# Optimization experiments

Hardware: AMD Instinct MI355X
Metric: run time of the kernel (lower is better)

The kernel has to match this reference:

```python
import jax, jax.numpy as jnp
import numpy as np

N_R, N_U, N_P = 40000, 30000, 30000
N = N_R + N_U + N_P
E = 1600000
NFEAT, NHID, NCLASS = 128, 128, 40


def setup_inputs() -> dict:
    key = jax.random.key(0)
    ks = jax.random.split(key, 12)
    s = 0.05
    return {
        "inputx_r": jax.random.normal(ks[0], (N_R, 5), jnp.float32),
        "inputx_u": jax.random.normal(ks[1], (N_U, 7), jnp.float32),
        "inputx_p": jax.random.normal(ks[2], (N_P, 6), jnp.float32),
        "edge_index": jax.random.randint(ks[3], (2, E), 0, N, jnp.int64)
            if jax.config.jax_enable_x64 else jax.random.randint(ks[3], (2, E), 0, N, jnp.int32),
        "W_r": jax.random.normal(ks[4], (5, NFEAT), jnp.float32) * s,
        "b_r": jax.random.normal(ks[5], (NFEAT,), jnp.float32) * s,
        "W_u": jax.random.normal(ks[6], (7, NFEAT), jnp.float32) * s,
        "b_u": jax.random.normal(ks[7], (NFEAT,), jnp.float32) * s,
        "W_p": jax.random.normal(ks[8], (6, NFEAT), jnp.float32) * s,
        "b_p": jax.random.normal(ks[9], (NFEAT,), jnp.float32) * s,
        "W1": jax.random.normal(ks[10], (NFEAT, NHID), jnp.float32) * s,
        "W2": jax.random.normal(ks[11], (NHID, NCLASS), jnp.float32) * s,
    }


def _gcn_conv(x, W, src, dst, num_nodes):
    # GCNConv(add_self_loops=False, normalize=False, bias=False):
    # out = A @ (x @ W), unit edge weights, aggregation at dst of source messages.
    h = x @ W                                      # [N, d_out]
    return jax.ops.segment_sum(h[src], dst, num_segments=num_nodes)


def reference(inputx_r, inputx_u, inputx_p, edge_index,
              W_r, b_r, W_u, b_u, W_p, b_p, W1, W2):
    # Segment-wise input projections (nums = [[N_R, N_R+N_U], [.,.], [.,.]]
    # with empty 2nd/3rd blocks; tail is the p-segment), then two GCN layers.
    x = jnp.concatenate([
        inputx_r @ W_r + b_r,   # nodes [0 : N_R]
        inputx_u @ W_u + b_u,   # nodes [N_R : N_R+N_U]
        inputx_p @ W_p + b_p,   # nodes [N_R+N_U : N]
    ], axis=0)                  # [N, NFEAT]
    src, dst = edge_index[0], edge_index[1]
    h = jax.nn.relu(_gcn_conv(x, W1, src, dst, N))   # gc1 + relu
    # dropout: inference (training=False) -> identity
    out = _gcn_conv(h, W2, src, dst, N)              # gc2
    return out
```

## Files before the change

### kernel.cpp

```cpp
#include <hip/hip_runtime.h>

constexpr int kNR = 40000;
constexpr int kNU = 30000;
constexpr int kNP = 30000;
constexpr int kN  = 100000;
constexpr int kE  = 1600000;
constexpr int kF  = 128;
constexpr int kC  = 40;
constexpr int kBN = 64;
constexpr int kNB = (kN + kBN - 1) / kBN;
constexpr int kNBp = 1600;
constexpr int kCH = 256;
constexpr int kCE = kE / kCH;
constexpr int kSlot = 2048;
constexpr int kPackB = 196;
constexpr int kSetupB = kPackB + 2;

typedef __attribute__((ext_vector_type(8))) short bf16x8;
typedef __attribute__((ext_vector_type(4))) float f32x4;

__device__ __forceinline__ float bf_to_f(unsigned short h) {
    union { unsigned int i; float f; } u; u.i = ((unsigned int)h) << 16; return u.f;
}
__device__ __forceinline__ unsigned short f_to_bf(float f) {
    union { unsigned int i; float f; } u; u.f = f;
    unsigned int r = u.i + 0x7FFFu + ((u.i >> 16) & 1u);
    return (unsigned short)(r >> 16);
}
__device__ __forceinline__ float2 bf2_to_f2(unsigned int p) {
    union { unsigned int i; float f; } lo, hi;
    lo.i = (p & 0xFFFFu) << 16;
    hi.i = p & 0xFFFF0000u;
    return make_float2(lo.f, hi.f);
}
__device__ __forceinline__ unsigned int pack_bf2(float a, float b) {
    return (unsigned int)f_to_bf(a) | ((unsigned int)f_to_bf(b) << 16);
}
__device__ __forceinline__ float ldf(const void* p, int i, int isbf) {
    return isbf ? bf_to_f(((const unsigned short*)p)[i]) : ((const float*)p)[i];
}
__device__ __forceinline__ int lde(const int* p, int i, int is64) {
    return is64 ? p[2 * i] : p[i];
}

__device__ __forceinline__ int sniff_isbf(const void* W1, int t, int* sh) {
    if (t < 64) {
        unsigned int wv = ((const unsigned int*)W1)[t];
        unsigned int ax = wv & 0x7FFFu;
        int pl = (ax == 0u) || (ax > 0x2000u && ax < 0x4000u);
        unsigned long long mk = __ballot(pl);
        if (t == 0) *sh = (__popcll(mk) >= 48) ? 1 : 0;
    }
    __syncthreads();
    return *sh;
}

__global__ void __launch_bounds__(512) gcn_setup(
        const void* __restrict__ xr, const void* __restrict__ xu, const void* __restrict__ xp,
        const void* __restrict__ Wr, const void* __restrict__ br,
        const void* __restrict__ Wu, const void* __restrict__ bu,
        const void* __restrict__ Wp, const void* __restrict__ bp,
        const void* __restrict__ W1, const void* __restrict__ W2,
        unsigned short* __restrict__ fwfrag, unsigned short* __restrict__ w2frag,
        uint4* __restrict__ xpack, int* __restrict__ gcnt) {
    __shared__ __align__(16) char smem[29696];
    __shared__ int sisbf;
    int t = threadIdx.x;
    int bx = blockIdx.x;
    int isbf = sniff_isbf(W1, t, &sisbf);
    if (bx < kPackB) {
        int n = bx * 512 + t;
        if (n >= kN) return;
        const void* base; int roff, d;
        if (n < kNR)            { base = xr; roff = n * 5;               d = 5; }
        else if (n < kNR + kNU) { base = xu; roff = (n - kNR) * 7;       d = 7; }
        else                    { base = xp; roff = (n - kNR - kNU) * 6; d = 6; }
        float f[8];
        #pragma unroll
        for (int i = 0; i < 8; i++) f[i] = (i < d) ? ldf(base, roff + i, isbf) : 0.f;
        uint4 u;
        u.x = pack_bf2(f[0], f[1]);  u.y = pack_bf2(f[2], f[3]);
        u.z = pack_bf2(f[4], f[5]);  u.w = pack_bf2(f[6], f[7]);
        xpack[n] = u;
    } else if (bx == kPackB) {
        float* sw   = (float*)smem;
        float* pacc = (float*)(smem + 10752);
        unsigned short* flds = (unsigned short*)(smem + 21504);
        for (int i = t; i < 21 * kF; i += 512) {
            int r = i >> 7, c = i & 127;
            float v;
            if (r < 5)        v = ldf(Wr, r * kF + c, isbf);
            else if (r < 12)  v = ldf(Wu, (r - 5) * kF + c, isbf);
            else if (r < 18)  v = ldf(Wp, (r - 12) * kF + c, isbf);
            else if (r == 18) v = ldf(br, c, isbf);
            else if (r == 19) v = ldf(bu, c, isbf);
            else              v = ldf(bp, c, isbf);
            sw[i] = v;
        }
        __syncthreads();
        {
            bool active = (t < 256);
            int j = t & 127, half = (t >> 7) & 1;
            float acc[21];
            #pragma unroll
            for (int r = 0; r < 21; r++) acc[r] = 0.f;
            if (active) {
                int k0 = half * 64, k1 = k0 + 64;
                for (int k = k0; k < k1; k++) {
                    float w1 = ldf(W1, k * kF + j, isbf);
                    #pragma unroll
                    for (int r = 0; r < 21; r++) acc[r] += sw[r * kF + k] * w1;
                }
            }
            if (active && half == 1) {
                #pragma unroll
                for (int r = 0; r < 21; r++) pacc[r * kF + j] = acc[r];
            }
            __syncthreads();
            if (active && half == 0) {
                #pragma unroll
                for (int r = 0; r < 21; r++) acc[r] += pacc[r * kF + j];
                unsigned short row[32];
                #pragma unroll
                for (int s = 0; s < 32; s++) row[s] = 0;
                #pragma unroll
                for (int i = 0; i < 5; i++) row[0  + i] = f_to_bf(acc[i]);
                #pragma unroll
                for (int i = 0; i < 7; i++) row[8  + i] = f_to_bf(acc[5 + i]);
                #pragma unroll
                for (int i = 0; i < 6; i++) row[16 + i] = f_to_bf(acc[12 + i]);
                row[24] = f_to_bf(acc[18]);  row[25] = f_to_bf(acc[19]);  row[26] = f_to_bf(acc[20]);
                #pragma unroll
                for (int s = 0; s < 32; s++) flds[j * 32 + s] = row[s];
            }
        }
        __syncthreads();
        for (int idx = t; idx < 8 * 64; idx += 512) {
            int t8 = idx >> 6, lane = idx & 63;
            int mm = lane & 15, q = lane >> 4;
            #pragma unroll
            for (int j = 0; j < 8; j++)
                fwfrag[idx * 8 + j] = flds[(16 * t8 + mm) * 32 + q * 8 + j];
        }
    } else {
        for (int i = t; i < kNBp; i += 512) gcnt[i] = 0;
        for (int idx = t; idx < 12 * 64; idx += 512) {
            int st = idx >> 6, lane = idx & 63;
            int s = st / 3, tt = st % 3;
            int mm = lane & 15, q = lane >> 4;
            int cls = 16 * tt + mm;
            #pragma unroll
            for (int j = 0; j < 8; j++) {
                int k = s * 32 + q * 8 + j;
                w2frag[idx * 8 + j] = (cls < kC) ? f_to_bf(ldf(W2, k * kC + cls, isbf))
                                                 : (unsigned short)0;
            }
        }
    }
}

__global__ void __launch_bounds__(1024) gcn_scatter(const int* __restrict__ ei,
                                                    int* __restrict__ gcnt,
                                                    unsigned int* __restrict__ slots) {
    __shared__ int hist[kNBp];
    __shared__ int cur[kNBp];
    __shared__ int sis64;
    int t = threadIdx.x;
    int blk = blockIdx.x;
    if (t < 64) {
        int v = ((const int*)ei)[2 * t + 1];
        unsigned long long mk = __ballot(v != 0);
        if (t == 0) sis64 = (mk == 0ull) ? 1 : 0;
    }
    for (int i = t; i < kNBp; i += 1024) hist[i] = 0;
    __syncthreads();
    int is64 = sis64;
    int e0 = blk * kCE, e1 = e0 + kCE;
    for (int eb = e0 + t; eb < e1; eb += 4096) {
        unsigned int d[4]; int ok[4];
        #pragma unroll
        for (int j = 0; j < 4; j++) {
            int e = eb + j * 1024;
            ok[j] = (e < e1);
            d[j] = ok[j] ? (unsigned int)lde(ei, kE + e, is64) : 0xFFFFFFFFu;
        }
        #pragma unroll
        for (int j = 0; j < 4; j++)
            if (d[j] < (unsigned int)kN) atomicAdd(&hist[d[j] >> 6], 1);
    }
    __syncthreads();
    int off = (blk * 401) % kNBp;
    for (int j = t; j < kNBp; j += 1024) {
        int i = j + off;
        if (i >= kNBp) i -= kNBp;
        int h = hist[i];
        cur[i] = (h > 0) ? atomicAdd(&gcnt[i], h) : 0;
    }
    __syncthreads();
    for (int eb = e0 + t; eb < e1; eb += 4096) {
        unsigned int d[4], s[4]; int ok[4];
        #pragma unroll
        for (int j = 0; j < 4; j++) {
            int e = eb + j * 1024;
            ok[j] = (e < e1);
            d[j] = ok[j] ? (unsigned int)lde(ei, kE + e, is64) : 0xFFFFFFFFu;
        }
        #pragma unroll
        for (int j = 0; j < 4; j++) {
            int e = eb + j * 1024;
            s[j] = ok[j] ? (unsigned int)lde(ei, e, is64) : 0u;
        }
        #pragma unroll
        for (int j = 0; j < 4; j++) {
            if (d[j] < (unsigned int)kN) {
                unsigned int sv = (s[j] < (unsigned int)kN) ? s[j] : 0u;
                int b = (int)(d[j] >> 6);
                int pos = atomicAdd(&cur[b], 1);
                if (pos < kSlot) slots[(size_t)b * kSlot + pos] = (sv << 6) | (d[j] & 63u);
            }
        }
    }
}

__global__ void __launch_bounds__(256) GCN_2190433321521_kernel(
        const unsigned int* __restrict__ slots,
        const int* __restrict__ gcnt,
        const uint4* __restrict__ xpack,
        const unsigned short* __restrict__ fwfrag,
        const unsigned short* __restrict__ w2frag,
        int* __restrict__ rpb,
        int* __restrict__ rpe,
        int* __restrict__ col,
        unsigned short* __restrict__ hw) {
    __shared__ __align__(16) char smem[25600];
    float*          agg_l  = (float*)smem;
    int*            cnt_l  = (int*)(smem + 7424);
    int*            strt_l = (int*)(smem + 7680);
    int*            cntv_l = (int*)(smem + 7936);
    unsigned int*   wst    = (unsigned int*)(smem + 8192);
    int*            col_l  = (int*)(smem + 16384);
    unsigned short* hbuf   = (unsigned short*)(smem + 8192);

    int b = blockIdx.x;
    int base = b * kBN;
    int nn = min(kBN, kN - base);
    int tid = threadIdx.x;

    if (tid < kBN) cnt_l[tid] = 0;
    __syncthreads();
    int p0 = b * kSlot;
    int m = min(gcnt[b], kSlot);
    int p1 = p0 + m;

    for (int ib = p0 + tid; ib < p1; ib += 1024) {
        unsigned int w[4]; int ok[4];
        #pragma unroll
        for (int j = 0; j < 4; j++) {
            int i = ib + j * 256;
            ok[j] = (i < p1);
            w[j] = ok[j] ? slots[i] : 0u;
        }
        #pragma unroll
        for (int j = 0; j < 4; j++) {
            int i = ib + j * 256;
            if (ok[j]) {
                wst[i - p0] = w[j];
                atomicAdd(&cnt_l[w[j] & 63u], 1);
            }
        }
    }
    __syncthreads();
    if (tid < 64) {
        int v = cnt_l[tid];
        int incl = v;
        #pragma unroll
        for (int o = 1; o < 64; o <<= 1) {
            int y = __shfl_up(incl, o, 64);
            if (tid >= o) incl += y;
        }
        int cursor = p0 + incl - v;
        cnt_l[tid]  = cursor;
        strt_l[tid] = cursor;
        cntv_l[tid] = v;
        if (tid < nn) { rpb[base + tid] = cursor; rpe[base + tid] = cursor + v; }
    }
    __syncthreads();

    for (int i = p0 + tid; i < p1; i += 256) {
        unsigned int w = wst[i - p0];
        unsigned int s = w >> 6;
        int dloc = (int)(w & 63u);
        int pos = atomicAdd(&cnt_l[dloc], 1);
        col_l[pos - p0] = (int)s;
    }
    __syncthreads();
    for (int i = tid; i < m; i += 256) col[p0 + i] = col_l[i];

    {
        int node = tid >> 2, j = tid & 3;
        float aR[8], aU[8], aP[8];
        #pragma unroll
        for (int i = 0; i < 8; i++) { aR[i] = 0.f; aU[i] = 0.f; aP[i] = 0.f; }
        float cR = 0.f, cU = 0.f, cP = 0.f;
        int start = strt_l[node] - p0;
        int c = cntv_l[node];
        for (int i = start + j; i < start + c; i += 4) {
            int s = col_l[i];
            uint4 u = xpack[s];
            float2 q0 = bf2_to_f2(u.x), q1 = bf2_to_f2(u.y);
            float2 q2 = bf2_to_f2(u.z), q3 = bf2_to_f2(u.w);
            if (s < kNR) {
                aR[0]+=q0.x; aR[1]+=q0.y; aR[2]+=q1.x; aR[3]+=q1.y;
                aR[4]+=q2.x; aR[5]+=q2.y; aR[6]+=q3.x; aR[7]+=q3.y; cR += 1.f;
            } else if (s < kNR + kNU) {
                aU[0]+=q0.x; aU[1]+=q0.y; aU[2]+=q1.x; aU[3]+=q1.y;
                aU[4]+=q2.x; aU[5]+=q2.y; aU[6]+=q3.x; aU[7]+=q3.y; cU += 1.f;
            } else {
                aP[0]+=q0.x; aP[1]+=q0.y; aP[2]+=q1.x; aP[3]+=q1.y;
                aP[4]+=q2.x; aP[5]+=q2.y; aP[6]+=q3.x; aP[7]+=q3.y; cP += 1.f;
            }
        }
        #pragma unroll
        for (int i = 0; i < 8; i++) {
            float v = aR[i];
            v += __shfl_xor(v, 1, 64);  v += __shfl_xor(v, 2, 64);
            if (j == 0) agg_l[node * 29 + i] = v;
        }
        #pragma unroll
        for (int i = 0; i < 8; i++) {
            float v = aU[i];
            v += __shfl_xor(v, 1, 64);  v += __shfl_xor(v, 2, 64);
            if (j == 0) agg_l[node * 29 + 8 + i] = v;
        }
        #pragma unroll
        for (int i = 0; i < 8; i++) {
            float v = aP[i];
            v += __shfl_xor(v, 1, 64);  v += __shfl_xor(v, 2, 64);
            if (j == 0) agg_l[node * 29 + 16 + i] = v;
        }
        float v = cR;
        v += __shfl_xor(v, 1, 64);  v += __shfl_xor(v, 2, 64);
        if (j == 0) agg_l[node * 29 + 24] = v;
        v = cU;
        v += __shfl_xor(v, 1, 64);  v += __shfl_xor(v, 2, 64);
        if (j == 0) agg_l[node * 29 + 25] = v;
        v = cP;
        v += __shfl_xor(v, 1, 64);  v += __shfl_xor(v, 2, 64);
        if (j == 0) agg_l[node * 29 + 26] = v;
    }
    __syncthreads();

    int wid = tid >> 6, lane = tid & 63;
    int mm = lane & 15, q = lane >> 4;
    int node = wid * 16 + mm;
    bf16x8 a1;
    #pragma unroll
    for (int j = 0; j < 8; j++) {
        int sl = q * 8 + j;
        a1[j] = (sl < 27) ? (short)f_to_bf(agg_l[node * 29 + sl]) : (short)0;
    }
    const bf16x8* fwf = (const bf16x8*)fwfrag;
    f32x4 c1[8];
    #pragma unroll
    for (int t = 0; t < 8; t++) {
        f32x4 z = {0.f, 0.f, 0.f, 0.f};
        c1[t] = __builtin_amdgcn_mfma_f32_16x16x32_bf16(a1, fwf[t * 64 + lane], z, 0, 0, 0);
    }
    unsigned short* hb = hbuf + wid * 16 * 136;
    #pragma unroll
    for (int t = 0; t < 8; t++) {
        #pragma unroll
        for (int r = 0; r < 4; r++)
            hb[(q * 4 + r) * 136 + 16 * t + mm] = f_to_bf(fmaxf(c1[t][r], 0.f));
    }
    const bf16x8* w2f = (const bf16x8*)w2frag;
    f32x4 c2[3];
    #pragma unroll
    for (int t = 0; t < 3; t++) { c2[t].x = 0.f; c2[t].y = 0.f; c2[t].z = 0.f; c2[t].w = 0.f; }
    #pragma unroll
    for (int s = 0; s < 4; s++) {
        bf16x8 a2 = *(const bf16x8*)&hb[mm * 136 + s * 32 + q * 8];
        #pragma unroll
        for (int t = 0; t < 3; t++)
            c2[t] = __builtin_amdgcn_mfma_f32_16x16x32_bf16(a2, w2f[(s * 3 + t) * 64 + lane],
                                                            c2[t], 0, 0, 0);
    }
    #pragma unroll
    for (int t = 0; t < 3; t++) {
        int cls = 16 * t + mm;
        if (cls < kC) {
            #pragma unroll
            for (int r = 0; r < 4; r++) {
                int n = base + wid * 16 + q * 4 + r;
                if (n < kN) hw[(size_t)n * kC + cls] = f_to_bf(c2[t][r]);
            }
        }
    }
}

__global__ void __launch_bounds__(256) gcn_gather2(const unsigned int* __restrict__ hw32,
                                                   const int* __restrict__ rpb,
                                                   const int* __restrict__ rpe,
                                                   const int* __restrict__ col,
                                                   unsigned int* __restrict__ out,
                                                   const void* __restrict__ W1) {
    __shared__ int sisbf;
    int t = threadIdx.x;
    int isbf = sniff_isbf(W1, t, &sisbf);
    int w = (blockIdx.x * 256 + t) >> 6;
    if (w >= kN) return;
    int lane = t & 63;
    int grp = lane / 10;
    int c2  = lane % 10;
    int beg = rpb[w], end = rpe[w];
    float f0 = 0.f, f1 = 0.f, f2 = 0.f, f3 = 0.f;
    if (grp < 6) {
        const uint2* hp = (const uint2*)hw32;
        int e = beg + grp;
        for (; e + 6 < end; e += 12) {
            int s0 = col[e], s1 = col[e + 6];
            uint2 v0 = hp[s0 * 10 + c2];
            uint2 v1 = hp[s1 * 10 + c2];
            float2 a0 = bf2_to_f2(v0.x), b0 = bf2_to_f2(v0.y);
            float2 a1 = bf2_to_f2(v1.x), b1 = bf2_to_f2(v1.y);
            f0 += a0.x + a1.x;  f1 += a0.y + a1.y;
            f2 += b0.x + b1.x;  f3 += b0.y + b1.y;
        }
        if (e < end) {
            uint2 v = hp[col[e] * 10 + c2];
            float2 a = bf2_to_f2(v.x), bb = bf2_to_f2(v.y);
            f0 += a.x; f1 += a.y; f2 += bb.x; f3 += bb.y;
        }
    }
    f0 += __shfl(f0, lane + 30, 64);
    f1 += __shfl(f1, lane + 30, 64);
    f2 += __shfl(f2, lane + 30, 64);
    f3 += __shfl(f3, lane + 30, 64);
    f0 += __shfl(f0, lane + 10, 64) + __shfl(f0, lane + 20, 64);
    f1 += __shfl(f1, lane + 10, 64) + __shfl(f1, lane + 20, 64);
    f2 += __shfl(f2, lane + 10, 64) + __shfl(f2, lane + 20, 64);
    f3 += __shfl(f3, lane + 10, 64) + __shfl(f3, lane + 20, 64);
    if (lane < 10) {
        if (isbf) {
            out[w * 20 + 2 * lane]     = pack_bf2(f0, f1);
            out[w * 20 + 2 * lane + 1] = pack_bf2(f2, f3);
        } else {
            float* of = (float*)out;
            of[w * 40 + 4 * lane]     = f0;
            of[w * 40 + 4 * lane + 1] = f1;
            of[w * 40 + 4 * lane + 2] = f2;
            of[w * 40 + 4 * lane + 3] = f3;
        }
    }
}

extern "C" void kernel_launch(void* const* d_in, const int* in_sizes, int n_in,
                              void* d_out, int out_size, void* d_ws, size_t ws_size,
                              hipStream_t stream) {
    const void* xr = d_in[0];
    const void* xu = d_in[1];
    const void* xp = d_in[2];
    const int*  ei = (const int*)d_in[3];
    const void* Wr = d_in[4];
    const void* br = d_in[5];
    const void* Wu = d_in[6];
    const void* bu = d_in[7];
    const void* Wp = d_in[8];
    const void* bp = d_in[9];
    const void* W1 = d_in[10];
    const void* W2 = d_in[11];
    (void)in_sizes; (void)n_in; (void)out_size; (void)ws_size;

    char* ws = (char*)d_ws;
    size_t off = 0;
    auto alloc = [&](size_t bytes) -> void* {
        void* p = (void*)(ws + off);
        off = (off + bytes + 255) & ~(size_t)255;
        return p;
    };
    int*            gcnt   = (int*)           alloc((size_t)kNBp * 4);
    unsigned short* fwfrag = (unsigned short*)alloc(8 * 64 * 8 * 2);
    unsigned short* w2frag = (unsigned short*)alloc(12 * 64 * 8 * 2);
    uint4*          xpack  = (uint4*)         alloc((size_t)kN * 16);
    unsigned int*   slots  = (unsigned int*)  alloc((size_t)kNB * kSlot * 4);
    int*            col    = (int*)           alloc((size_t)kNB * kSlot * 4);
    int*            rpb    = (int*)           alloc((size_t)kN * 4);
    int*            rpe    = (int*)           alloc((size_t)kN * 4);
    unsigned short* hwb    = (unsigned short*)alloc((size_t)kN * kC * 2);

    gcn_setup<<<kSetupB, 512, 0, stream>>>(xr, xu, xp, Wr, br, Wu, bu, Wp, bp, W1, W2,
                                           fwfrag, w2frag, xpack, gcnt);
    gcn_scatter<<<kCH, 1024, 0, stream>>>(ei, gcnt, slots);
    GCN_2190433321521_kernel<<<kNB, 256, 0, stream>>>(slots, gcnt, xpack, fwfrag, w2frag,
                                                      rpb, rpe, col, hwb);
    gcn_gather2<<<(kN * 64 + 255) / 256, 256, 0, stream>>>((const unsigned int*)hwb, rpb, rpe,
                                                           col, (unsigned int*)d_out, W1);
}
```

Measured before the change: 190.7 us.

## Merge setup and scatter kernels, stage layer-2 outputs in LDS, prefetch gather indices

Folds the setup kernel and the edge-scatter kernel into one launch with 1024-thread blocks, and moves the counter zeroing to a memset. This removes a kernel boundary and lets the scatter run alongside the packing work. The main kernel now writes its layer-2 bf16 outputs to shared memory first, then stores them to global memory as contiguous 32-bit words. The second gather preloads four column indices up front to expose more memory-level parallelism. The cost is an extra memset launch, extra block syncs, and halving the scatter block count, which may reduce parallelism in the edge pass.

```diff
diff --git a/kernel.cpp b/kernel.cpp
--- a/kernel.cpp
+++ b/kernel.cpp
@@ -10,11 +10,14 @@
 constexpr int kBN = 64;
 constexpr int kNB = (kN + kBN - 1) / kBN;
 constexpr int kNBp = 1600;
-constexpr int kCH = 256;
-constexpr int kCE = kE / kCH;
 constexpr int kSlot = 2048;
-constexpr int kPackB = 196;
-constexpr int kSetupB = kPackB + 2;
+constexpr int kPackB = 98;
+constexpr int kFuseB = kPackB;
+constexpr int kW2B   = kPackB + 1;
+constexpr int kScat0 = kPackB + 2;
+constexpr int kScatB = 128;
+constexpr int kCE    = kE / kScatB;
+constexpr int kPrepB = kScat0 + kScatB;
 
 typedef __attribute__((ext_vector_type(8))) short bf16x8;
 typedef __attribute__((ext_vector_type(4))) float f32x4;
@@ -55,21 +58,23 @@
     return *sh;
 }
 
-__global__ void __launch_bounds__(512) gcn_setup(
+__global__ void __launch_bounds__(1024) gcn_prep(
         const void* __restrict__ xr, const void* __restrict__ xu, const void* __restrict__ xp,
         const void* __restrict__ Wr, const void* __restrict__ br,
         const void* __restrict__ Wu, const void* __restrict__ bu,
         const void* __restrict__ Wp, const void* __restrict__ bp,
         const void* __restrict__ W1, const void* __restrict__ W2,
+        const int* __restrict__ ei,
         unsigned short* __restrict__ fwfrag, unsigned short* __restrict__ w2frag,
-        uint4* __restrict__ xpack, int* __restrict__ gcnt) {
+        uint4* __restrict__ xpack, int* __restrict__ gcnt,
+        unsigned int* __restrict__ slots) {
     __shared__ __align__(16) char smem[29696];
-    __shared__ int sisbf;
+    __shared__ int sflag;
     int t = threadIdx.x;
     int bx = blockIdx.x;
-    int isbf = sniff_isbf(W1, t, &sisbf);
     if (bx < kPackB) {
-        int n = bx * 512 + t;
+        int isbf = sniff_isbf(W1, t, &sflag);
+        int n = bx * 1024 + t;
         if (n >= kN) return;
         const void* base; int roff, d;
         if (n < kNR)            { base = xr; roff = n * 5;               d = 5; }
@@ -82,11 +87,12 @@
         u.x = pack_bf2(f[0], f[1]);  u.y = pack_bf2(f[2], f[3]);
         u.z = pack_bf2(f[4], f[5]);  u.w = pack_bf2(f[6], f[7]);
         xpack[n] = u;
-    } else if (bx == kPackB) {
+    } else if (bx == kFuseB) {
+        int isbf = sniff_isbf(W1, t, &sflag);
         float* sw   = (float*)smem;
         float* pacc = (float*)(smem + 10752);
         unsigned short* flds = (unsigned short*)(smem + 21504);
-        for (int i = t; i < 21 * kF; i += 512) {
+        for (int i = t; i < 21 * kF; i += 1024) {
             int r = i >> 7, c = i & 127;
             float v;
             if (r < 5)        v = ldf(Wr, r * kF + c, isbf);
@@ -135,16 +141,16 @@
             }
         }
         __syncthreads();
-        for (int idx = t; idx < 8 * 64; idx += 512) {
+        for (int idx = t; idx < 8 * 64; idx += 1024) {
             int t8 = idx >> 6, lane = idx & 63;
             int mm = lane & 15, q = lane >> 4;
             #pragma unroll
             for (int j = 0; j < 8; j++)
                 fwfrag[idx * 8 + j] = flds[(16 * t8 + mm) * 32 + q * 8 + j];
         }
-    } else {
-        for (int i = t; i < kNBp; i += 512) gcnt[i] = 0;
-        for (int idx = t; idx < 12 * 64; idx += 512) {
+    } else if (bx == kW2B) {
+        int isbf = sniff_isbf(W1, t, &sflag);
+        for (int idx = t; idx < 12 * 64; idx += 1024) {
             int st = idx >> 6, lane = idx & 63;
             int s = st / 3, tt = st % 3;
             int mm = lane & 15, q = lane >> 4;
@@ -156,67 +162,59 @@
                                                  : (unsigned short)0;
             }
         }
-    }
-}
-
-__global__ void __launch_bounds__(1024) gcn_scatter(const int* __restrict__ ei,
-                                                    int* __restrict__ gcnt,
-                                                    unsigned int* __restrict__ slots) {
-    __shared__ int hist[kNBp];
-    __shared__ int cur[kNBp];
-    __shared__ int sis64;
-    int t = threadIdx.x;
-    int blk = blockIdx.x;
-    if (t < 64) {
-        int v = ((const int*)ei)[2 * t + 1];
-        unsigned long long mk = __ballot(v != 0);
-        if (t == 0) sis64 = (mk == 0ull) ? 1 : 0;
-    }
-    for (int i = t; i < kNBp; i += 1024) hist[i] = 0;
-    __syncthreads();
-    int is64 = sis64;
-    int e0 = blk * kCE, e1 = e0 + kCE;
-    for (int eb = e0 + t; eb < e1; eb += 4096) {
-        unsigned int d[4]; int ok[4];
-        #pragma unroll
-        for (int j = 0; j < 4; j++) {
-            int e = eb + j * 1024;
-            ok[j] = (e < e1);
-            d[j] = ok[j] ? (unsigned int)lde(ei, kE + e, is64) : 0xFFFFFFFFu;
-        }
-        #pragma unroll
-        for (int j = 0; j < 4; j++)
-            if (d[j] < (unsigned int)kN) atomicAdd(&hist[d[j] >> 6], 1);
-    }
-    __syncthreads();
-    int off = (blk * 401) % kNBp;
-    for (int j = t; j < kNBp; j += 1024) {
-        int i = j + off;
-        if (i >= kNBp) i -= kNBp;
-        int h = hist[i];
-        cur[i] = (h > 0) ? atomicAdd(&gcnt[i], h) : 0;
-    }
-    __syncthreads();
-    for (int eb = e0 + t; eb < e1; eb += 4096) {
-        unsigned int d[4], s[4]; int ok[4];
-        #pragma unroll
-        for (int j = 0; j < 4; j++) {
-            int e = eb + j * 1024;
-            ok[j] = (e < e1);
-            d[j] = ok[j] ? (unsigned int)lde(ei, kE + e, is64) : 0xFFFFFFFFu;
-        }
-        #pragma unroll
-        for (int j = 0; j < 4; j++) {
-            int e = eb + j * 1024;
-            s[j] = ok[j] ? (unsigned int)lde(ei, e, is64) : 0u;
-        }
-        #pragma unroll
-        for (int j = 0; j < 4; j++) {
-            if (d[j] < (unsigned int)kN) {
-                unsigned int sv = (s[j] < (unsigned int)kN) ? s[j] : 0u;
-                int b = (int)(d[j] >> 6);
-                int pos = atomicAdd(&cur[b], 1);
-                if (pos < kSlot) slots[(size_t)b * kSlot + pos] = (sv << 6) | (d[j] & 63u);
+    } else {
+        int* hist = (int*)smem;
+        int* cur  = (int*)(smem + 6400);
+        if (t < 64) {
+            int v = ((const int*)ei)[2 * t + 1];
+            unsigned long long mk = __ballot(v != 0);
+            if (t == 0) sflag = (mk == 0ull) ? 1 : 0;
+        }
+        for (int i = t; i < kNBp; i += 1024) hist[i] = 0;
+        __syncthreads();
+        int is64 = sflag;
+        int blk = bx - kScat0;
+        int e0 = blk * kCE, e1 = e0 + kCE;
+        for (int eb = e0 + t; eb < e1; eb += 4096) {
+            unsigned int d[4];
+            #pragma unroll
+            for (int j = 0; j < 4; j++) {
+                int e = eb + j * 1024;
+                d[j] = (e < e1) ? (unsigned int)lde(ei, kE + e, is64) : 0xFFFFFFFFu;
+            }
+            #pragma unroll
+            for (int j = 0; j < 4; j++)
+                if (d[j] < (unsigned int)kN) atomicAdd(&hist[d[j] >> 6], 1);
+        }
+        __syncthreads();
+        int off = (blk * 401) % kNBp;
+        for (int j = t; j < kNBp; j += 1024) {
+            int i = j + off;
+            if (i >= kNBp) i -= kNBp;
+            int h = hist[i];
+            cur[i] = (h > 0) ? atomicAdd(&gcnt[i], h) : 0;
+        }
+        __syncthreads();
+        for (int eb = e0 + t; eb < e1; eb += 4096) {
+            unsigned int d[4], s[4];
+            #pragma unroll
+            for (int j = 0; j < 4; j++) {
+                int e = eb + j * 1024;
+                d[j] = (e < e1) ? (unsigned int)lde(ei, kE + e, is64) : 0xFFFFFFFFu;
+            }
+            #pragma unroll
+            for (int j = 0; j < 4; j++) {
+                int e = eb + j * 1024;
+                s[j] = (e < e1) ? (unsigned int)lde(ei, e, is64) : 0u;
+            }
+            #pragma unroll
+            for (int j = 0; j < 4; j++) {
+                if (d[j] < (unsigned int)kN) {
+                    unsigned int sv = (s[j] < (unsigned int)kN) ? s[j] : 0u;
+                    int b = (int)(d[j] >> 6);
+                    int pos = atomicAdd(&cur[b], 1);
+                    if (pos < kSlot) slots[(size_t)b * kSlot + pos] = (sv << 6) | (d[j] & 63u);
+                }
             }
         }
     }
@@ -240,6 +238,7 @@
     unsigned int*   wst    = (unsigned int*)(smem + 8192);
     int*            col_l  = (int*)(smem + 16384);
     unsigned short* hbuf   = (unsigned short*)(smem + 8192);
+    unsigned short* cst    = (unsigned short*)smem;
 
     int b = blockIdx.x;
     int base = b * kBN;
@@ -359,6 +358,7 @@
         int sl = q * 8 + j;
         a1[j] = (sl < 27) ? (short)f_to_bf(agg_l[node * 29 + sl]) : (short)0;
     }
+    __syncthreads();
     const bf16x8* fwf = (const bf16x8*)fwfrag;
     f32x4 c1[8];
     #pragma unroll
@@ -390,11 +390,16 @@
         int cls = 16 * t + mm;
         if (cls < kC) {
             #pragma unroll
-            for (int r = 0; r < 4; r++) {
-                int n = base + wid * 16 + q * 4 + r;
-                if (n < kN) hw[(size_t)n * kC + cls] = f_to_bf(c2[t][r]);
-            }
-        }
+            for (int r = 0; r < 4; r++)
+                cst[(wid * 16 + q * 4 + r) * kC + cls] = f_to_bf(c2[t][r]);
+        }
+    }
+    __syncthreads();
+    {
+        int tot = nn * (kC / 2);
+        const unsigned int* cs32 = (const unsigned int*)cst;
+        unsigned int* ho = (unsigned int*)(hw + (size_t)base * kC);
+        for (int i = tid; i < tot; i += 256) ho[i] = cs32[i];
     }
 }
 
@@ -411,23 +416,39 @@
     if (w >= kN) return;
     int lane = t & 63;
     int grp = lane / 10;
-    int c2  = lane % 10;
+    int cp  = lane % 10;
     int beg = rpb[w], end = rpe[w];
     float f0 = 0.f, f1 = 0.f, f2 = 0.f, f3 = 0.f;
     if (grp < 6) {
         const uint2* hp = (const uint2*)hw32;
         int e = beg + grp;
-        for (; e + 6 < end; e += 12) {
-            int s0 = col[e], s1 = col[e + 6];
-            uint2 v0 = hp[s0 * 10 + c2];
-            uint2 v1 = hp[s1 * 10 + c2];
-            float2 a0 = bf2_to_f2(v0.x), b0 = bf2_to_f2(v0.y);
-            float2 a1 = bf2_to_f2(v1.x), b1 = bf2_to_f2(v1.y);
-            f0 += a0.x + a1.x;  f1 += a0.y + a1.y;
-            f2 += b0.x + b1.x;  f3 += b0.y + b1.y;
-        }
-        if (e < end) {
-            uint2 v = hp[col[e] * 10 + c2];
+        int c0 = (e      < end) ? col[e]      : -1;
+        int c1 = (e + 6  < end) ? col[e + 6]  : -1;
+        int c2 = (e + 12 < end) ? col[e + 12] : -1;
+        int c3 = (e + 18 < end) ? col[e + 18] : -1;
+        if (c0 >= 0) {
+            uint2 v = hp[c0 * 10 + cp];
+            float2 a = bf2_to_f2(v.x), bb = bf2_to_f2(v.y);
+            f0 += a.x; f1 += a.y; f2 += bb.x; f3 += bb.y;
+        }
+        if (c1 >= 0) {
+            uint2 v = hp[c1 * 10 + cp];
+            float2 a = bf2_to_f2(v.x), bb = bf2_to_f2(v.y);
+            f0 += a.x; f1 += a.y; f2 += bb.x; f3 += bb.y;
+        }
+        if (c2 >= 0) {
+            uint2 v = hp[c2 * 10 + cp];
+            float2 a = bf2_to_f2(v.x), bb = bf2_to_f2(v.y);
+            f0 += a.x; f1 += a.y; f2 += bb.x; f3 += bb.y;
+        }
+        if (c3 >= 0) {
+            uint2 v = hp[c3 * 10 + cp];
+            float2 a = bf2_to_f2(v.x), bb = bf2_to_f2(v.y);
+            f0 += a.x; f1 += a.y; f2 += bb.x; f3 += bb.y;
+        }
+        for (e += 24; e < end; e += 6) {
+            int s = col[e];
+            uint2 v = hp[s * 10 + cp];
             float2 a = bf2_to_f2(v.x), bb = bf2_to_f2(v.y);
             f0 += a.x; f1 += a.y; f2 += bb.x; f3 += bb.y;
         }
@@ -488,9 +509,9 @@
     int*            rpe    = (int*)           alloc((size_t)kN * 4);
     unsigned short* hwb    = (unsigned short*)alloc((size_t)kN * kC * 2);
 
-    gcn_setup<<<kSetupB, 512, 0, stream>>>(xr, xu, xp, Wr, br, Wu, bu, Wp, bp, W1, W2,
-                                           fwfrag, w2frag, xpack, gcnt);
-    gcn_scatter<<<kCH, 1024, 0, stream>>>(ei, gcnt, slots);
+    hipMemsetAsync(gcnt, 0, (size_t)kNBp * 4, stream);
+    gcn_prep<<<kPrepB, 1024, 0, stream>>>(xr, xu, xp, Wr, br, Wu, bu, Wp, bp, W1, W2,
+                                          ei, fwfrag, w2frag, xpack, gcnt, slots);
     GCN_2190433321521_kernel<<<kNB, 256, 0, stream>>>(slots, gcnt, xpack, fwfrag, w2frag,
                                                       rpb, rpe, col, hwb);
     gcn_gather2<<<(kN * 64 + 255) / 256, 256, 0, stream>>>((const unsigned int*)hwb, rpb, rpe,
```

New measurement: 176.7 us. 1.08x faster.
